# Optimization experiments

Measured on AMD Instinct MI355X. Metric: run time of the kernel, lower is better.

Reference implementation:

```python
import jax, jax.numpy as jnp
import numpy as np

B, T, F = 512, 98, 40
DIM, DEPTH, HEADS, DHEAD, MLP, NCLS = 192, 12, 3, 64, 768, 35
INNER = HEADS * DHEAD  # 192
N = T + 1  # cls token prepended
EPS = 1e-5


def _ln(x, g, b):
    m = jnp.mean(x, axis=-1, keepdims=True)
    v = jnp.mean(jnp.square(x - m), axis=-1, keepdims=True)
    return (x - m) * jax.lax.rsqrt(v + EPS) * g + b


def setup_inputs() -> dict:
    key = jax.random.key(0)
    ks = jax.random.split(key, 16)
    s = 0.02
    inp = {
        "img": jax.random.normal(ks[0], (B, T, F), jnp.float32),
        "lin_w": jax.random.normal(ks[1], (F, DIM), jnp.float32) * s,
        "g_feat": jax.random.normal(ks[2], (1, 1, DIM), jnp.float32),
        "pos_emb": jax.random.normal(ks[3], (1, N, DIM), jnp.float32),
        "ln1_g": jnp.ones((DEPTH, DIM), jnp.float32),
        "ln1_b": jnp.zeros((DEPTH, DIM), jnp.float32),
        "ln2_g": jnp.ones((DEPTH, DIM), jnp.float32),
        "ln2_b": jnp.zeros((DEPTH, DIM), jnp.float32),
        "qkv_w": jax.random.normal(ks[4], (DEPTH, DIM, 3 * INNER), jnp.float32) * s,
        "out_w": jax.random.normal(ks[5], (DEPTH, INNER, DIM), jnp.float32) * s,
        "out_b": jnp.zeros((DEPTH, DIM), jnp.float32),
        "ff1_w": jax.random.normal(ks[6], (DEPTH, DIM, MLP), jnp.float32) * s,
        "ff1_b": jnp.zeros((DEPTH, MLP), jnp.float32),
        "ff2_w": jax.random.normal(ks[7], (DEPTH, MLP, DIM), jnp.float32) * s,
        "ff2_b": jnp.zeros((DEPTH, DIM), jnp.float32),
        "head_ln_g": jnp.ones((DIM,), jnp.float32),
        "head_ln_b": jnp.zeros((DIM,), jnp.float32),
        "head_w": jax.random.normal(ks[8], (DIM, NCLS), jnp.float32) * s,
        "head_b": jnp.zeros((NCLS,), jnp.float32),
    }
    return inp


def reference(img, lin_w, g_feat, pos_emb, ln1_g, ln1_b, ln2_g, ln2_b,
              qkv_w, out_w, out_b, ff1_w, ff1_b, ff2_w, ff2_b,
              head_ln_g, head_ln_b, head_w, head_b):
    scale = DHEAD ** -0.5
    x = img @ lin_w  # [B, T, DIM]
    cls = jnp.broadcast_to(g_feat, (B, 1, DIM))
    x = jnp.concatenate([cls, x], axis=1) + pos_emb  # [B, N, DIM]

    for i in range(DEPTH):
        # --- attention (manual softmax, post-norm residual) ---
        qkv = x @ qkv_w[i]  # [B, N, 3*INNER]
        q, k, v = jnp.split(qkv, 3, axis=-1)
        rs = lambda t: t.reshape(B, N, HEADS, DHEAD).transpose(0, 2, 1, 3)
        q, k, v = rs(q), rs(k), rs(v)  # [B, H, N, D]
        dots = jnp.einsum('bhid,bhjd->bhij', q, k) * scale
        attn = jax.nn.softmax(dots, axis=-1)
        o = jnp.einsum('bhij,bhjd->bhid', attn, v)
        o = o.transpose(0, 2, 1, 3).reshape(B, N, INNER)
        o = o @ out_w[i] + out_b[i]
        x = _ln(o + x, ln1_g[i], ln1_b[i])
        # --- feedforward (exact GELU) ---
        h = jax.nn.gelu(x @ ff1_w[i] + ff1_b[i], approximate=False)
        f = h @ ff2_w[i] + ff2_b[i]
        x = _ln(f + x, ln2_g[i], ln2_b[i])

    x = x[:, 0]  # cls pooling
    x = _ln(x, head_ln_g, head_ln_b)
    return x @ head_w + head_b  # [B, NCLS]
```

## Files before the change

### kernel.cpp

```cpp
#include <hip/hip_runtime.h>

typedef unsigned short u16;

#define DIMM   192
#define DEPTH  12
#define NHEAD  3
#define MLPD   768
#define NCLS   35
#define NTOK   99
#define TIMG   98
#define FIMG   40
#define NBATCH 512
#define MT     7

#define XS_S 200
#define QH_S 72
#define VT_S 136
#define P_S  136
#define XS0  0
#define QH0  22400
#define KH0  30464
#define VT0  38528
#define P0   47232
#define RR_BYTE 124928
#define SMEM_BYTES 128512

typedef __attribute__((ext_vector_type(8))) __bf16 bf8;
typedef __attribute__((ext_vector_type(4))) float  f4;

__device__ __forceinline__ float b2f(u16 u){
  union { float f; unsigned u; } v; v.u = ((unsigned)u) << 16; return v.f;
}
__device__ __forceinline__ u16 f2b(float f){
  __bf16 h = (__bf16)f;
  union { __bf16 h; u16 u; } v; v.h = h;
  return v.u;
}
__device__ __forceinline__ f4 mm(bf8 a, bf8 b, f4 c){
  return __builtin_amdgcn_mfma_f32_16x16x32_bf16(a, b, c, 0, 0, 0);
}
__device__ __forceinline__ float gelu_f(float x){
  float z = x * 0.7071067811865476f;
  float az = fabsf(z);
  float t = 1.0f / (1.0f + 0.3275911f * az);
  float poly = ((((1.061405429f*t - 1.453152027f)*t + 1.421413741f)*t
                 - 0.284496736f)*t + 0.254829592f)*t;
  float erfv = 1.0f - poly * __expf(-az*az);
  erfv = (z < 0.0f) ? -erfv : erfv;
  return 0.5f * x * (1.0f + erfv);
}

extern "C" __global__ void permw(const float* __restrict__ src, u16* __restrict__ dst,
                                 int total, int KT, int NT, int realK, int Ndim){
  int i = blockIdx.x * 256 + threadIdx.x;
  if (i >= total) return;
  int j = i & 7, l = (i >> 3) & 63;
  int rest = i >> 9;
  int kt = rest % KT; rest /= KT;
  int nt = rest % NT; int layer = rest / NT;
  int k = kt*32 + (l>>4)*8 + j;
  int n = nt*16 + (l&15);
  float v = (k < realK) ? src[((size_t)layer*realK + k)*Ndim + n] : 0.0f;
  union { float f; unsigned u; } w; w.f = v;
  unsigned r = w.u + 0x7FFFu + ((w.u >> 16) & 1u);
  dst[i] = (u16)(r >> 16);
}

extern "C" __global__
__attribute__((amdgpu_flat_work_group_size(512,512), amdgpu_waves_per_eu(2,2)))
void vit_main(
    const float* __restrict__ img,   const float* __restrict__ g_feat,
    const float* __restrict__ pos_emb,
    const float* __restrict__ ln1_g, const float* __restrict__ ln1_b,
    const float* __restrict__ ln2_g, const float* __restrict__ ln2_b,
    const float* __restrict__ out_b, const float* __restrict__ ff1_b,
    const float* __restrict__ ff2_b,
    const float* __restrict__ hln_g, const float* __restrict__ hln_b,
    const float* __restrict__ head_w, const float* __restrict__ head_b,
    const u16* __restrict__ wlin, const u16* __restrict__ wqkv,
    const u16* __restrict__ wout, const u16* __restrict__ wff1,
    const u16* __restrict__ wff2,
    float* __restrict__ out)
{
  extern __shared__ __align__(16) u16 sm[];
  float* rowred = (float*)((char*)sm + RR_BYTE);
  const int tid  = threadIdx.x;
  const int lane = tid & 63;
  const int wv   = tid >> 6;
  const int wm   = wv >> 2;
  const int wn   = wv & 3;
  const int lg   = lane >> 4;
  const int lr   = lane & 15;
  const int b    = blockIdx.x;

  u16* const pA  = sm + XS0 + (wm*64 + lr)*XS_S + lg*8;
  u16* const pH  = sm + QH0 + (wm*64 + lr)*XS_S + lg*8;
  u16* const pOA = sm + QH0 + (wm*64 + lr)*QH_S + lg*8;
  u16* const pQS = sm + QH0 + (wm*64 + lg*4)*QH_S + wn*16 + lr;
  u16* const pVS = sm + VT0 + (wn*16 + lr)*VT_S + wm*64 + lg*4;
  u16* const pQA = sm + QH0 + (wv*16 + lr)*QH_S + lg*8;
  u16* const pKB = sm + KH0 + lr*QH_S + lg*8;
  u16* const pPS = sm + P0  + (wv*16 + lg*4)*P_S + lr;
  u16* const pPA = sm + P0  + (wv*16 + lr)*P_S + lg*8;
  u16* const pVB = sm + VT0 + lr*VT_S + lg*8;
  u16* const pOS = sm + QH0 + (wv*16 + lg*4)*QH_S + lr;
  u16* const pXE = sm + XS0 + (wm*64 + lg*4)*XS_S + wn*48 + lr;
  float* const pRR = rowred + (wm*64 + lg*4)*8;
  float* const pRS = pRR + wn*2;

  for (int i = tid; i < SMEM_BYTES/4; i += 512) ((unsigned*)sm)[i] = 0u;
  __syncthreads();

  const f4 zero4 = {0.f,0.f,0.f,0.f};

  auto epilogue_ln = [&](f4 (&acc)[4][3],
                         const float* gptr, const float* bptr, const float* biasptr){
    float gg[3], bb[3], ob[3];
#pragma unroll
    for (int nt = 0; nt < 3; ++nt) {
      int c = wn*48 + nt*16 + lr;
      gg[nt] = gptr[c]; bb[nt] = bptr[c]; ob[nt] = biasptr[c];
    }
#pragma unroll
    for (int mi = 0; mi < 4; ++mi) {
      if (mi < 3 || wm == 0) {
#pragma unroll
        for (int r = 0; r < 4; ++r) {
          float s1 = 0.f, s2 = 0.f;
#pragma unroll
          for (int nt = 0; nt < 3; ++nt) {
            float v = acc[mi][nt][r] + ob[nt] + b2f(pXE[(mi*16+r)*XS_S + nt*16]);
            acc[mi][nt][r] = v;
            s1 += v; s2 += v*v;
          }
          s1 += __shfl_xor(s1,1); s2 += __shfl_xor(s2,1);
          s1 += __shfl_xor(s1,2); s2 += __shfl_xor(s2,2);
          s1 += __shfl_xor(s1,4); s2 += __shfl_xor(s2,4);
          s1 += __shfl_xor(s1,8); s2 += __shfl_xor(s2,8);
          if (lr == 0) {
            pRS[(mi*16+r)*8 + 0] = s1;
            pRS[(mi*16+r)*8 + 1] = s2;
          }
        }
      }
    }
    __syncthreads();
#pragma unroll
    for (int mi = 0; mi < 4; ++mi) {
      if (mi < 3 || wm == 0) {
#pragma unroll
        for (int r = 0; r < 4; ++r) {
          float4 q0 = *(const float4*)&pRR[(mi*16+r)*8];
          float4 q1 = *(const float4*)&pRR[(mi*16+r)*8 + 4];
          float S1 = q0.x + q0.z + q1.x + q1.z;
          float S2 = q0.y + q0.w + q1.y + q1.w;
          float mean = S1 * (1.0f/DIMM);
          float var  = S2 * (1.0f/DIMM) - mean*mean;
          float rs = rsqrtf(var + 1e-5f);
          int row = wm*64 + mi*16 + lg*4 + r;
          if (row < NTOK) {
#pragma unroll
            for (int nt = 0; nt < 3; ++nt) {
              float y = (acc[mi][nt][r] - mean)*rs*gg[nt] + bb[nt];
              pXE[(mi*16+r)*XS_S + nt*16] = f2b(y);
            }
          }
        }
      }
    }
    __syncthreads();
  };

  const float* imgb = img + (size_t)b * (TIMG*FIMG);
  for (int i = tid; i < TIMG*FIMG; i += 512) {
    int r = i / FIMG, c = i - r*FIMG;
    sm[QH0 + (r+1)*QH_S + c] = f2b(imgb[i]);
  }
  __syncthreads();
  {
    const u16* wl = wlin + (size_t)(wn*3)*2*512 + lane*8;
    bf8 Bf[3][2];
#pragma unroll
    for (int nt = 0; nt < 3; ++nt)
#pragma unroll
      for (int kt = 0; kt < 2; ++kt)
        Bf[nt][kt] = *(const bf8*)&wl[(nt*2+kt)*512];
#pragma unroll
    for (int mi = 0; mi < 4; ++mi) {
      if (mi < 3 || wm == 0) {
        bf8 Af[2];
#pragma unroll
        for (int kt = 0; kt < 2; ++kt)
          Af[kt] = *(const bf8*)&pOA[mi*16*QH_S + kt*32];
#pragma unroll
        for (int nt = 0; nt < 3; ++nt) {
          f4 a = zero4;
#pragma unroll
          for (int kt = 0; kt < 2; ++kt) a = mm(Af[kt], Bf[nt][kt], a);
          int col = wn*48 + nt*16 + lr;
#pragma unroll
          for (int r = 0; r < 4; ++r) {
            int row = wm*64 + mi*16 + lg*4 + r;
            if (row < NTOK) {
              float v = a[r] + pos_emb[row*DIMM + col] + (row==0 ? g_feat[col] : 0.f);
              pXE[(mi*16+r)*XS_S + nt*16] = f2b(v);
            }
          }
        }
      }
    }
  }
  __syncthreads();

  for (int L = 0; L < DEPTH; ++L) {
    const u16* wq = wqkv + (size_t)L*36*6*512;
    f4 oacc[4][3];
#pragma unroll
    for (int mi = 0; mi < 4; ++mi)
#pragma unroll
      for (int nt = 0; nt < 3; ++nt) oacc[mi][nt] = zero4;

    for (int h = 0; h < NHEAD; ++h) {
      {
        const u16* wp = wq + ((size_t)(h*4 + wn)*6)*512 + lane*8;
        bf8 B[6];
#pragma unroll
        for (int kt = 0; kt < 6; ++kt) B[kt] = *(const bf8*)&wp[kt*512];
#pragma unroll
        for (int mi = 0; mi < 4; ++mi) {
          if (mi < 3 || wm == 0) {
            bf8 Af[6];
#pragma unroll
            for (int kt = 0; kt < 6; ++kt)
              Af[kt] = *(const bf8*)&pA[mi*16*XS_S + kt*32];
            f4 a = zero4;
#pragma unroll
            for (int kt = 0; kt < 6; ++kt) a = mm(Af[kt], B[kt], a);
#pragma unroll
            for (int r = 0; r < 4; ++r)
              pQS[(mi*16+r)*QH_S] = f2b(a[r]*0.125f);
          }
        }
      }
      {
        const u16* wp = wq + ((size_t)(12 + h*4 + wn)*6)*512 + lane*8;
        bf8 B[6];
#pragma unroll
        for (int kt = 0; kt < 6; ++kt) B[kt] = *(const bf8*)&wp[kt*512];
#pragma unroll
        for (int mi = 0; mi < 4; ++mi) {
          if (mi < 3 || wm == 0) {
            bf8 Af[6];
#pragma unroll
            for (int kt = 0; kt < 6; ++kt)
              Af[kt] = *(const bf8*)&pA[mi*16*XS_S + kt*32];
            f4 a = zero4;
#pragma unroll
            for (int kt = 0; kt < 6; ++kt) a = mm(Af[kt], B[kt], a);
#pragma unroll
            for (int r = 0; r < 4; ++r)
              pQS[(KH0-QH0) + (mi*16+r)*QH_S] = f2b(a[r]);
          }
        }
      }
      {
        const u16* wp = wq + ((size_t)(24 + h*4 + wn)*6)*512 + lane*8;
        bf8 B[6];
#pragma unroll
        for (int kt = 0; kt < 6; ++kt) B[kt] = *(const bf8*)&wp[kt*512];
#pragma unroll
        for (int mi = 0; mi < 4; ++mi) {
          if (mi < 3 || wm == 0) {
            bf8 Af[6];
#pragma unroll
            for (int kt = 0; kt < 6; ++kt)
              Af[kt] = *(const bf8*)&pA[mi*16*XS_S + kt*32];
            f4 a = zero4;
#pragma unroll
            for (int kt = 0; kt < 6; ++kt) a = mm(Af[kt], B[kt], a);
#pragma unroll
            for (int r = 0; r < 4; ++r)
              pVS[mi*16 + r] = f2b(a[r]);
          }
        }
      }
      __syncthreads();

      if (wv < MT) {
        bf8 Aq[2];
#pragma unroll
        for (int ks = 0; ks < 2; ++ks)
          Aq[ks] = *(const bf8*)&pQA[ks*32];
        f4 s[7];
#pragma unroll
        for (int kt = 0; kt < 7; ++kt) {
          f4 a = zero4;
#pragma unroll
          for (int ks = 0; ks < 2; ++ks) {
            bf8 Bk2 = *(const bf8*)&pKB[kt*16*QH_S + ks*32];
            a = mm(Aq[ks], Bk2, a);
          }
          s[kt] = a;
        }
#pragma unroll
        for (int r = 0; r < 4; ++r) {
          float m = s[0][r];
#pragma unroll
          for (int kt = 1; kt < 6; ++kt) m = fmaxf(m, s[kt][r]);
          m = fmaxf(m, (lr < 3) ? s[6][r] : -1e30f);
          m = fmaxf(m, __shfl_xor(m, 1));
          m = fmaxf(m, __shfl_xor(m, 2));
          m = fmaxf(m, __shfl_xor(m, 4));
          m = fmaxf(m, __shfl_xor(m, 8));
          float p[7]; float sum = 0.f;
#pragma unroll
          for (int kt = 0; kt < 6; ++kt) { p[kt] = __expf(s[kt][r] - m); sum += p[kt]; }
          p[6] = (lr < 3) ? __expf(s[6][r] - m) : 0.f;
          sum += p[6];
          sum += __shfl_xor(sum, 1);
          sum += __shfl_xor(sum, 2);
          sum += __shfl_xor(sum, 4);
          sum += __shfl_xor(sum, 8);
          float inv = 1.0f / sum;
#pragma unroll
          for (int kt = 0; kt < 7; ++kt)
            pPS[r*P_S + kt*16] = f2b(p[kt]*inv);
        }
        asm volatile("" ::: "memory");
        bf8 Ap[4];
#pragma unroll
        for (int ks = 0; ks < 4; ++ks)
          Ap[ks] = *(const bf8*)&pPA[ks*32];
#pragma unroll
        for (int nt = 0; nt < 4; ++nt) {
          f4 a = zero4;
#pragma unroll
          for (int ks = 0; ks < 4; ++ks) {
            bf8 Bv2 = *(const bf8*)&pVB[nt*16*VT_S + ks*32];
            a = mm(Ap[ks], Bv2, a);
          }
#pragma unroll
          for (int r = 0; r < 4; ++r)
            pOS[r*QH_S + nt*16] = f2b(a[r]);
        }
      }
      __syncthreads();

      {
        const u16* wp = wout + (((size_t)(L*12 + wn*3)*6) + h*2)*512 + lane*8;
        bf8 Bo[3][2];
#pragma unroll
        for (int nt = 0; nt < 3; ++nt)
#pragma unroll
          for (int ks = 0; ks < 2; ++ks)
            Bo[nt][ks] = *(const bf8*)&wp[(nt*6 + ks)*512];
#pragma unroll
        for (int mi = 0; mi < 4; ++mi) {
          if (mi < 3 || wm == 0) {
            bf8 Ao[2];
#pragma unroll
            for (int ks = 0; ks < 2; ++ks)
              Ao[ks] = *(const bf8*)&pOA[mi*16*QH_S + ks*32];
#pragma unroll
            for (int nt = 0; nt < 3; ++nt)
#pragma unroll
              for (int ks = 0; ks < 2; ++ks)
                oacc[mi][nt] = mm(Ao[ks], Bo[nt][ks], oacc[mi][nt]);
          }
        }
      }
      __syncthreads();
    }

    epilogue_ln(oacc, ln1_g + L*DIMM, ln1_b + L*DIMM, out_b + L*DIMM);

    f4 facc[4][3];
#pragma unroll
    for (int mi = 0; mi < 4; ++mi)
#pragma unroll
      for (int nt = 0; nt < 3; ++nt) facc[mi][nt] = zero4;

    for (int blk = 0; blk < 4; ++blk) {
      {
        const u16* wp = wff1 + ((size_t)(L*48 + blk*12 + wn*3)*6)*512 + lane*8;
        const float* fbp = ff1_b + L*MLPD + blk*192 + wn*48 + lr;
#pragma unroll
        for (int nt = 0; nt < 3; ++nt) {
          bf8 B[6];
#pragma unroll
          for (int kt = 0; kt < 6; ++kt) B[kt] = *(const bf8*)&wp[(nt*6+kt)*512];
          float fb = fbp[nt*16];
#pragma unroll
          for (int mi = 0; mi < 4; ++mi) {
            if (mi < 3 || wm == 0) {
              bf8 Af[6];
#pragma unroll
              for (int kt = 0; kt < 6; ++kt)
                Af[kt] = *(const bf8*)&pA[mi*16*XS_S + kt*32];
              f4 a = zero4;
#pragma unroll
              for (int kt = 0; kt < 6; ++kt) a = mm(Af[kt], B[kt], a);
#pragma unroll
              for (int r = 0; r < 4; ++r)
                pXE[(QH0-XS0) + (mi*16+r)*XS_S + nt*16] = f2b(gelu_f(a[r] + fb));
            }
          }
        }
      }
      __syncthreads();
      {
        const u16* wp = wff2 + ((size_t)(L*12 + wn*3)*24 + blk*6)*512 + lane*8;
#pragma unroll
        for (int nt = 0; nt < 3; ++nt) {
          bf8 B[6];
#pragma unroll
          for (int kt = 0; kt < 6; ++kt) B[kt] = *(const bf8*)&wp[(nt*24+kt)*512];
#pragma unroll
          for (int mi = 0; mi < 4; ++mi) {
            if (mi < 3 || wm == 0) {
              bf8 Ah[6];
#pragma unroll
              for (int kt = 0; kt < 6; ++kt)
                Ah[kt] = *(const bf8*)&pH[mi*16*XS_S + kt*32];
#pragma unroll
              for (int kt = 0; kt < 6; ++kt)
                facc[mi][nt] = mm(Ah[kt], B[kt], facc[mi][nt]);
            }
          }
        }
      }
      __syncthreads();
    }

    epilogue_ln(facc, ln2_g + L*DIMM, ln2_b + L*DIMM, ff2_b + L*DIMM);
  }

  float* yv = rowred;
  if (wv == 0) {
    float x0 = b2f(sm[XS0 + lane]);
    float x1 = b2f(sm[XS0 + 64 + lane]);
    float x2 = b2f(sm[XS0 + 128 + lane]);
    float s1 = x0+x1+x2;
    float s2 = x0*x0 + x1*x1 + x2*x2;
#pragma unroll
    for (int d = 1; d < 64; d <<= 1) { s1 += __shfl_xor(s1, d); s2 += __shfl_xor(s2, d); }
    float mean = s1*(1.0f/DIMM), var = s2*(1.0f/DIMM) - mean*mean;
    float rs = rsqrtf(var + 1e-5f);
    yv[lane]      = (x0-mean)*rs*hln_g[lane]      + hln_b[lane];
    yv[64+lane]   = (x1-mean)*rs*hln_g[64+lane]   + hln_b[64+lane];
    yv[128+lane]  = (x2-mean)*rs*hln_g[128+lane]  + hln_b[128+lane];
  }
  __syncthreads();
  if (tid < NCLS) {
    float acc = head_b[tid];
    for (int k = 0; k < DIMM; ++k) acc += yv[k] * head_w[k*NCLS + tid];
    out[(size_t)b*NCLS + tid] = acc;
  }
}

extern "C" void kernel_launch(void* const* d_in, const int* in_sizes, int n_in,
                              void* d_out, int out_size, void* d_ws, size_t ws_size,
                              hipStream_t stream) {
  const float* img    = (const float*)d_in[0];
  const float* lin_w  = (const float*)d_in[1];
  const float* g_feat = (const float*)d_in[2];
  const float* pos_emb= (const float*)d_in[3];
  const float* ln1_g  = (const float*)d_in[4];
  const float* ln1_b  = (const float*)d_in[5];
  const float* ln2_g  = (const float*)d_in[6];
  const float* ln2_b  = (const float*)d_in[7];
  const float* qkv_w  = (const float*)d_in[8];
  const float* out_w  = (const float*)d_in[9];
  const float* out_b  = (const float*)d_in[10];
  const float* ff1_w  = (const float*)d_in[11];
  const float* ff1_b  = (const float*)d_in[12];
  const float* ff2_w  = (const float*)d_in[13];
  const float* ff2_b  = (const float*)d_in[14];
  const float* hln_g  = (const float*)d_in[15];
  const float* hln_b  = (const float*)d_in[16];
  const float* head_w = (const float*)d_in[17];
  const float* head_b = (const float*)d_in[18];

  u16* ws   = (u16*)d_ws;
  u16* wlin = ws;
  u16* wqkv = wlin + 12288;
  u16* wout = wqkv + 1327104;
  u16* wff1 = wout + 442368;
  u16* wff2 = wff1 + 1769472;

  struct PermArgs { const float* src; u16* dst; int layers, Kdim, Ndim, realK; };
  const PermArgs pa[5] = {
    { lin_w, wlin, 1, 64, 192, 40 },
    { qkv_w, wqkv, 12, 192, 576, 192 },
    { out_w, wout, 12, 192, 192, 192 },
    { ff1_w, wff1, 12, 192, 768, 192 },
    { ff2_w, wff2, 12, 768, 192, 768 },
  };
  for (int i = 0; i < 5; ++i) {
    int total = pa[i].layers * (pa[i].Ndim/16) * (pa[i].Kdim/32) * 512;
    hipLaunchKernelGGL(permw, dim3((total + 255)/256), dim3(256), 0, stream,
                       pa[i].src, pa[i].dst, total, pa[i].Kdim/32, pa[i].Ndim/16,
                       pa[i].realK, pa[i].Ndim);
  }

  hipFuncSetAttribute(reinterpret_cast<const void*>(vit_main),
                      hipFuncAttributeMaxDynamicSharedMemorySize, SMEM_BYTES);

  hipLaunchKernelGGL(vit_main, dim3(NBATCH), dim3(512), SMEM_BYTES, stream,
                     img, g_feat, pos_emb, ln1_g, ln1_b, ln2_g, ln2_b,
                     out_b, ff1_b, ff2_b, hln_g, hln_b, head_w, head_b,
                     wlin, wqkv, wout, wff1, wff2, (float*)d_out);
}
```

Baseline: 1.573 ms.

## Split row tiles into two segments to cut accumulator register pressure

```diff
diff --git a/kernel.cpp b/kernel.cpp
--- a/kernel.cpp
+++ b/kernel.cpp
@@ -27,6 +27,7 @@
 
 typedef __attribute__((ext_vector_type(8))) __bf16 bf8;
 typedef __attribute__((ext_vector_type(4))) float  f4;
+typedef __attribute__((ext_vector_type(2))) unsigned u32x2;
 
 __device__ __forceinline__ float b2f(u16 u){
   union { float f; unsigned u; } v; v.u = ((unsigned)u) << 16; return v.f;
@@ -113,8 +114,8 @@
 
   const f4 zero4 = {0.f,0.f,0.f,0.f};
 
-  auto epilogue_ln = [&](f4 (&acc)[4][3],
-                         const float* gptr, const float* bptr, const float* biasptr){
+  auto epi_seg = [&](f4 (&acc)[2][3], int seg,
+                     const float* gptr, const float* bptr, const float* biasptr){
     float gg[3], bb[3], ob[3];
 #pragma unroll
     for (int nt = 0; nt < 3; ++nt) {
@@ -122,15 +123,16 @@
       gg[nt] = gptr[c]; bb[nt] = bptr[c]; ob[nt] = biasptr[c];
     }
 #pragma unroll
-    for (int mi = 0; mi < 4; ++mi) {
-      if (mi < 3 || wm == 0) {
+    for (int mi2 = 0; mi2 < 2; ++mi2) {
+      if (seg*2 + mi2 < 3 || wm == 0) {
 #pragma unroll
         for (int r = 0; r < 4; ++r) {
+          int ro = seg*32 + mi2*16 + r;
           float s1 = 0.f, s2 = 0.f;
 #pragma unroll
           for (int nt = 0; nt < 3; ++nt) {
-            float v = acc[mi][nt][r] + ob[nt] + b2f(pXE[(mi*16+r)*XS_S + nt*16]);
-            acc[mi][nt][r] = v;
+            float v = acc[mi2][nt][r] + ob[nt] + b2f(pXE[ro*XS_S + nt*16]);
+            acc[mi2][nt][r] = v;
             s1 += v; s2 += v*v;
           }
           s1 += __shfl_xor(s1,1); s2 += __shfl_xor(s2,1);
@@ -138,31 +140,32 @@
           s1 += __shfl_xor(s1,4); s2 += __shfl_xor(s2,4);
           s1 += __shfl_xor(s1,8); s2 += __shfl_xor(s2,8);
           if (lr == 0) {
-            pRS[(mi*16+r)*8 + 0] = s1;
-            pRS[(mi*16+r)*8 + 1] = s2;
+            pRS[ro*8 + 0] = s1;
+            pRS[ro*8 + 1] = s2;
           }
         }
       }
     }
     __syncthreads();
 #pragma unroll
-    for (int mi = 0; mi < 4; ++mi) {
-      if (mi < 3 || wm == 0) {
+    for (int mi2 = 0; mi2 < 2; ++mi2) {
+      if (seg*2 + mi2 < 3 || wm == 0) {
 #pragma unroll
         for (int r = 0; r < 4; ++r) {
-          float4 q0 = *(const float4*)&pRR[(mi*16+r)*8];
-          float4 q1 = *(const float4*)&pRR[(mi*16+r)*8 + 4];
+          int ro = seg*32 + mi2*16 + r;
+          float4 q0 = *(const float4*)&pRR[ro*8];
+          float4 q1 = *(const float4*)&pRR[ro*8 + 4];
           float S1 = q0.x + q0.z + q1.x + q1.z;
           float S2 = q0.y + q0.w + q1.y + q1.w;
           float mean = S1 * (1.0f/DIMM);
           float var  = S2 * (1.0f/DIMM) - mean*mean;
           float rs = rsqrtf(var + 1e-5f);
-          int row = wm*64 + mi*16 + lg*4 + r;
+          int row = wm*64 + ro + lg*4;
           if (row < NTOK) {
 #pragma unroll
             for (int nt = 0; nt < 3; ++nt) {
-              float y = (acc[mi][nt][r] - mean)*rs*gg[nt] + bb[nt];
-              pXE[(mi*16+r)*XS_S + nt*16] = f2b(y);
+              float y = (acc[mi2][nt][r] - mean)*rs*gg[nt] + bb[nt];
+              pXE[ro*XS_S + nt*16] = f2b(y);
             }
           }
         }
@@ -214,74 +217,71 @@
 
   for (int L = 0; L < DEPTH; ++L) {
     const u16* wq = wqkv + (size_t)L*36*6*512;
-    f4 oacc[4][3];
-#pragma unroll
-    for (int mi = 0; mi < 4; ++mi)
-#pragma unroll
-      for (int nt = 0; nt < 3; ++nt) oacc[mi][nt] = zero4;
+    f4 oacc0[2][3], oacc1[2][3];
+#pragma unroll
+    for (int mi2 = 0; mi2 < 2; ++mi2)
+#pragma unroll
+      for (int nt = 0; nt < 3; ++nt) { oacc0[mi2][nt] = zero4; oacc1[mi2][nt] = zero4; }
 
     for (int h = 0; h < NHEAD; ++h) {
-      {
-        const u16* wp = wq + ((size_t)(h*4 + wn)*6)*512 + lane*8;
-        bf8 B[6];
-#pragma unroll
-        for (int kt = 0; kt < 6; ++kt) B[kt] = *(const bf8*)&wp[kt*512];
-#pragma unroll
-        for (int mi = 0; mi < 4; ++mi) {
-          if (mi < 3 || wm == 0) {
+      const u16* wpq = wq + ((size_t)(      h*4 + wn)*6)*512 + lane*8;
+      const u16* wpk = wq + ((size_t)(12 + h*4 + wn)*6)*512 + lane*8;
+      const u16* wpv = wq + ((size_t)(24 + h*4 + wn)*6)*512 + lane*8;
+#pragma unroll
+      for (int seg = 0; seg < 2; ++seg) {
+#pragma unroll
+        for (int mi2 = 0; mi2 < 2; ++mi2) {
+          if (seg*2 + mi2 < 3 || wm == 0) {
+            const int ro = seg*32 + mi2*16;
             bf8 Af[6];
 #pragma unroll
             for (int kt = 0; kt < 6; ++kt)
-              Af[kt] = *(const bf8*)&pA[mi*16*XS_S + kt*32];
-            f4 a = zero4;
-#pragma unroll
-            for (int kt = 0; kt < 6; ++kt) a = mm(Af[kt], B[kt], a);
-#pragma unroll
-            for (int r = 0; r < 4; ++r)
-              pQS[(mi*16+r)*QH_S] = f2b(a[r]*0.125f);
-          }
-        }
-      }
-      {
-        const u16* wp = wq + ((size_t)(12 + h*4 + wn)*6)*512 + lane*8;
-        bf8 B[6];
-#pragma unroll
-        for (int kt = 0; kt < 6; ++kt) B[kt] = *(const bf8*)&wp[kt*512];
-#pragma unroll
-        for (int mi = 0; mi < 4; ++mi) {
-          if (mi < 3 || wm == 0) {
-            bf8 Af[6];
-#pragma unroll
-            for (int kt = 0; kt < 6; ++kt)
-              Af[kt] = *(const bf8*)&pA[mi*16*XS_S + kt*32];
-            f4 a = zero4;
-#pragma unroll
-            for (int kt = 0; kt < 6; ++kt) a = mm(Af[kt], B[kt], a);
-#pragma unroll
-            for (int r = 0; r < 4; ++r)
-              pQS[(KH0-QH0) + (mi*16+r)*QH_S] = f2b(a[r]);
-          }
-        }
-      }
-      {
-        const u16* wp = wq + ((size_t)(24 + h*4 + wn)*6)*512 + lane*8;
-        bf8 B[6];
-#pragma unroll
-        for (int kt = 0; kt < 6; ++kt) B[kt] = *(const bf8*)&wp[kt*512];
-#pragma unroll
-        for (int mi = 0; mi < 4; ++mi) {
-          if (mi < 3 || wm == 0) {
-            bf8 Af[6];
-#pragma unroll
-            for (int kt = 0; kt < 6; ++kt)
-              Af[kt] = *(const bf8*)&pA[mi*16*XS_S + kt*32];
-            f4 a = zero4;
-#pragma unroll
-            for (int kt = 0; kt < 6; ++kt) a = mm(Af[kt], B[kt], a);
-#pragma unroll
-            for (int r = 0; r < 4; ++r)
-              pVS[mi*16 + r] = f2b(a[r]);
-          }
+              Af[kt] = *(const bf8*)&pA[ro*XS_S + kt*32];
+            {
+              bf8 B[6];
+#pragma unroll
+              for (int kt = 0; kt < 6; ++kt) B[kt] = *(const bf8*)&wpq[kt*512];
+              f4 aA = zero4, aB = zero4;
+#pragma unroll
+              for (int k = 0; k < 3; ++k) aA = mm(Af[k], B[k], aA);
+#pragma unroll
+              for (int k = 0; k < 3; ++k) aB = mm(Af[3+k], B[3+k], aB);
+              f4 a = aA + aB;
+#pragma unroll
+              for (int r = 0; r < 4; ++r)
+                pQS[(ro+r)*QH_S] = f2b(a[r]*0.125f);
+            }
+            {
+              bf8 B[6];
+#pragma unroll
+              for (int kt = 0; kt < 6; ++kt) B[kt] = *(const bf8*)&wpk[kt*512];
+              f4 aA = zero4, aB = zero4;
+#pragma unroll
+              for (int k = 0; k < 3; ++k) aA = mm(Af[k], B[k], aA);
+#pragma unroll
+              for (int k = 0; k < 3; ++k) aB = mm(Af[3+k], B[3+k], aB);
+              f4 a = aA + aB;
+#pragma unroll
+              for (int r = 0; r < 4; ++r)
+                pQS[(KH0-QH0) + (ro+r)*QH_S] = f2b(a[r]);
+            }
+            {
+              bf8 B[6];
+#pragma unroll
+              for (int kt = 0; kt < 6; ++kt) B[kt] = *(const bf8*)&wpv[kt*512];
+              f4 aA = zero4, aB = zero4;
+#pragma unroll
+              for (int k = 0; k < 3; ++k) aA = mm(Af[k], B[k], aA);
+#pragma unroll
+              for (int k = 0; k < 3; ++k) aB = mm(Af[3+k], B[3+k], aB);
+              f4 a = aA + aB;
+              u32x2 pk;
+              pk.x = (unsigned)f2b(a[0]) | ((unsigned)f2b(a[1]) << 16);
+              pk.y = (unsigned)f2b(a[2]) | ((unsigned)f2b(a[3]) << 16);
+              *(u32x2*)(pVS + ro) = pk;
+            }
+          }
+          asm volatile("" ::: "memory");
         }
       }
       __syncthreads();
@@ -364,75 +364,88 @@
 #pragma unroll
             for (int nt = 0; nt < 3; ++nt)
 #pragma unroll
-              for (int ks = 0; ks < 2; ++ks)
-                oacc[mi][nt] = mm(Ao[ks], Bo[nt][ks], oacc[mi][nt]);
+              for (int ks = 0; ks < 2; ++ks) {
+                if (mi < 2) oacc0[mi  ][nt] = mm(Ao[ks], Bo[nt][ks], oacc0[mi  ][nt]);
+                else        oacc1[mi-2][nt] = mm(Ao[ks], Bo[nt][ks], oacc1[mi-2][nt]);
+              }
           }
         }
       }
       __syncthreads();
     }
 
-    epilogue_ln(oacc, ln1_g + L*DIMM, ln1_b + L*DIMM, out_b + L*DIMM);
-
-    f4 facc[4][3];
-#pragma unroll
-    for (int mi = 0; mi < 4; ++mi)
-#pragma unroll
-      for (int nt = 0; nt < 3; ++nt) facc[mi][nt] = zero4;
-
-    for (int blk = 0; blk < 4; ++blk) {
-      {
-        const u16* wp = wff1 + ((size_t)(L*48 + blk*12 + wn*3)*6)*512 + lane*8;
-        const float* fbp = ff1_b + L*MLPD + blk*192 + wn*48 + lr;
-#pragma unroll
-        for (int nt = 0; nt < 3; ++nt) {
-          bf8 B[6];
-#pragma unroll
-          for (int kt = 0; kt < 6; ++kt) B[kt] = *(const bf8*)&wp[(nt*6+kt)*512];
-          float fb = fbp[nt*16];
-#pragma unroll
-          for (int mi = 0; mi < 4; ++mi) {
-            if (mi < 3 || wm == 0) {
+    epi_seg(oacc0, 0, ln1_g + L*DIMM, ln1_b + L*DIMM, out_b + L*DIMM);
+    epi_seg(oacc1, 1, ln1_g + L*DIMM, ln1_b + L*DIMM, out_b + L*DIMM);
+
+#pragma unroll
+    for (int seg = 0; seg < 2; ++seg) {
+      f4 facc[2][3];
+#pragma unroll
+      for (int mi2 = 0; mi2 < 2; ++mi2)
+#pragma unroll
+        for (int nt = 0; nt < 3; ++nt) facc[mi2][nt] = zero4;
+
+      for (int blk = 0; blk < 4; ++blk) {
+        {
+          const u16* wp = wff1 + ((size_t)(L*48 + blk*12 + wn*3)*6)*512 + lane*8;
+          const float* fbp = ff1_b + L*MLPD + blk*192 + wn*48 + lr;
+#pragma unroll
+          for (int mi2 = 0; mi2 < 2; ++mi2) {
+            if (seg*2 + mi2 < 3 || wm == 0) {
+              const int ro = seg*32 + mi2*16;
               bf8 Af[6];
 #pragma unroll
               for (int kt = 0; kt < 6; ++kt)
-                Af[kt] = *(const bf8*)&pA[mi*16*XS_S + kt*32];
-              f4 a = zero4;
-#pragma unroll
-              for (int kt = 0; kt < 6; ++kt) a = mm(Af[kt], B[kt], a);
-#pragma unroll
-              for (int r = 0; r < 4; ++r)
-                pXE[(QH0-XS0) + (mi*16+r)*XS_S + nt*16] = f2b(gelu_f(a[r] + fb));
-            }
-          }
-        }
-      }
-      __syncthreads();
-      {
-        const u16* wp = wff2 + ((size_t)(L*12 + wn*3)*24 + blk*6)*512 + lane*8;
-#pragma unroll
-        for (int nt = 0; nt < 3; ++nt) {
-          bf8 B[6];
-#pragma unroll
-          for (int kt = 0; kt < 6; ++kt) B[kt] = *(const bf8*)&wp[(nt*24+kt)*512];
-#pragma unroll
-          for (int mi = 0; mi < 4; ++mi) {
-            if (mi < 3 || wm == 0) {
+                Af[kt] = *(const bf8*)&pA[ro*XS_S + kt*32];
+#pragma unroll
+              for (int nt = 0; nt < 3; ++nt) {
+                bf8 B[6];
+#pragma unroll
+                for (int kt = 0; kt < 6; ++kt) B[kt] = *(const bf8*)&wp[(nt*6+kt)*512];
+                float fb = fbp[nt*16];
+                f4 aA = zero4, aB = zero4;
+#pragma unroll
+                for (int k = 0; k < 3; ++k) aA = mm(Af[k], B[k], aA);
+#pragma unroll
+                for (int k = 0; k < 3; ++k) aB = mm(Af[3+k], B[3+k], aB);
+                f4 a = aA + aB;
+#pragma unroll
+                for (int r = 0; r < 4; ++r)
+                  pXE[(QH0-XS0) + (ro+r)*XS_S + nt*16] = f2b(gelu_f(a[r] + fb));
+                asm volatile("" ::: "memory");
+              }
+            }
+          }
+        }
+        __syncthreads();
+        {
+          const u16* wp = wff2 + ((size_t)(L*12 + wn*3)*24 + blk*6)*512 + lane*8;
+#pragma unroll
+          for (int mi2 = 0; mi2 < 2; ++mi2) {
+            if (seg*2 + mi2 < 3 || wm == 0) {
+              const int ro = seg*32 + mi2*16;
               bf8 Ah[6];
 #pragma unroll
               for (int kt = 0; kt < 6; ++kt)
-                Ah[kt] = *(const bf8*)&pH[mi*16*XS_S + kt*32];
-#pragma unroll
-              for (int kt = 0; kt < 6; ++kt)
-                facc[mi][nt] = mm(Ah[kt], B[kt], facc[mi][nt]);
-            }
-          }
-        }
-      }
-      __syncthreads();
+                Ah[kt] = *(const bf8*)&pH[ro*XS_S + kt*32];
+#pragma unroll
+              for (int nt = 0; nt < 3; ++nt) {
+                bf8 B[6];
+#pragma unroll
+                for (int kt = 0; kt < 6; ++kt) B[kt] = *(const bf8*)&wp[(nt*24+kt)*512];
+#pragma unroll
+                for (int kt = 0; kt < 6; ++kt)
+                  facc[mi2][nt] = mm(Ah[kt], B[kt], facc[mi2][nt]);
+                asm volatile("" ::: "memory");
+              }
+            }
+          }
+        }
+        __syncthreads();
+      }
+
+      epi_seg(facc, seg, ln2_g + L*DIMM, ln2_b + L*DIMM, ff2_b + L*DIMM);
     }
-
-    epilogue_ln(facc, ln2_g + L*DIMM, ln2_b + L*DIMM, ff2_b + L*DIMM);
   }
 
   float* yv = rowred;
```

After: 1.995 ms. 26.8% more time.

## Double workgroup to 1024 threads, halve per-wave row tiles, split MFMA chains

Applied to the files above, without the earlier changes.

```diff
diff --git a/kernel.cpp b/kernel.cpp
--- a/kernel.cpp
+++ b/kernel.cpp
@@ -27,6 +27,7 @@
 
 typedef __attribute__((ext_vector_type(8))) __bf16 bf8;
 typedef __attribute__((ext_vector_type(4))) float  f4;
+typedef __attribute__((ext_vector_type(2))) unsigned u32x2;
 
 __device__ __forceinline__ float b2f(u16 u){
   union { float f; unsigned u; } v; v.u = ((unsigned)u) << 16; return v.f;
@@ -67,7 +68,7 @@
 }
 
 extern "C" __global__
-__attribute__((amdgpu_flat_work_group_size(512,512), amdgpu_waves_per_eu(2,2)))
+__attribute__((amdgpu_flat_work_group_size(1024,1024), amdgpu_waves_per_eu(4,4)))
 void vit_main(
     const float* __restrict__ img,   const float* __restrict__ g_feat,
     const float* __restrict__ pos_emb,
@@ -93,27 +94,27 @@
   const int lr   = lane & 15;
   const int b    = blockIdx.x;
 
-  u16* const pA  = sm + XS0 + (wm*64 + lr)*XS_S + lg*8;
-  u16* const pH  = sm + QH0 + (wm*64 + lr)*XS_S + lg*8;
-  u16* const pOA = sm + QH0 + (wm*64 + lr)*QH_S + lg*8;
-  u16* const pQS = sm + QH0 + (wm*64 + lg*4)*QH_S + wn*16 + lr;
-  u16* const pVS = sm + VT0 + (wn*16 + lr)*VT_S + wm*64 + lg*4;
+  u16* const pA  = sm + XS0 + (wm*32 + lr)*XS_S + lg*8;
+  u16* const pH  = sm + QH0 + (wm*32 + lr)*XS_S + lg*8;
+  u16* const pOA = sm + QH0 + (wm*32 + lr)*QH_S + lg*8;
+  u16* const pQS = sm + QH0 + (wm*32 + lg*4)*QH_S + wn*16 + lr;
+  u16* const pVS = sm + VT0 + (wn*16 + lr)*VT_S + wm*32 + lg*4;
   u16* const pQA = sm + QH0 + (wv*16 + lr)*QH_S + lg*8;
   u16* const pKB = sm + KH0 + lr*QH_S + lg*8;
   u16* const pPS = sm + P0  + (wv*16 + lg*4)*P_S + lr;
   u16* const pPA = sm + P0  + (wv*16 + lr)*P_S + lg*8;
   u16* const pVB = sm + VT0 + lr*VT_S + lg*8;
   u16* const pOS = sm + QH0 + (wv*16 + lg*4)*QH_S + lr;
-  u16* const pXE = sm + XS0 + (wm*64 + lg*4)*XS_S + wn*48 + lr;
-  float* const pRR = rowred + (wm*64 + lg*4)*8;
+  u16* const pXE = sm + XS0 + (wm*32 + lg*4)*XS_S + wn*48 + lr;
+  float* const pRR = rowred + (wm*32 + lg*4)*8;
   float* const pRS = pRR + wn*2;
 
-  for (int i = tid; i < SMEM_BYTES/4; i += 512) ((unsigned*)sm)[i] = 0u;
+  for (int i = tid; i < SMEM_BYTES/4; i += 1024) ((unsigned*)sm)[i] = 0u;
   __syncthreads();
 
   const f4 zero4 = {0.f,0.f,0.f,0.f};
 
-  auto epilogue_ln = [&](f4 (&acc)[4][3],
+  auto epilogue_ln = [&](f4 (&acc)[2][3],
                          const float* gptr, const float* bptr, const float* biasptr){
     float gg[3], bb[3], ob[3];
 #pragma unroll
@@ -122,14 +123,15 @@
       gg[nt] = gptr[c]; bb[nt] = bptr[c]; ob[nt] = biasptr[c];
     }
 #pragma unroll
-    for (int mi = 0; mi < 4; ++mi) {
-      if (mi < 3 || wm == 0) {
+    for (int mi = 0; mi < 2; ++mi) {
+      if (wm < 3 || mi == 0) {
 #pragma unroll
         for (int r = 0; r < 4; ++r) {
+          int ro = mi*16 + r;
           float s1 = 0.f, s2 = 0.f;
 #pragma unroll
           for (int nt = 0; nt < 3; ++nt) {
-            float v = acc[mi][nt][r] + ob[nt] + b2f(pXE[(mi*16+r)*XS_S + nt*16]);
+            float v = acc[mi][nt][r] + ob[nt] + b2f(pXE[ro*XS_S + nt*16]);
             acc[mi][nt][r] = v;
             s1 += v; s2 += v*v;
           }
@@ -138,31 +140,32 @@
           s1 += __shfl_xor(s1,4); s2 += __shfl_xor(s2,4);
           s1 += __shfl_xor(s1,8); s2 += __shfl_xor(s2,8);
           if (lr == 0) {
-            pRS[(mi*16+r)*8 + 0] = s1;
-            pRS[(mi*16+r)*8 + 1] = s2;
+            pRS[ro*8 + 0] = s1;
+            pRS[ro*8 + 1] = s2;
           }
         }
       }
     }
     __syncthreads();
 #pragma unroll
-    for (int mi = 0; mi < 4; ++mi) {
-      if (mi < 3 || wm == 0) {
+    for (int mi = 0; mi < 2; ++mi) {
+      if (wm < 3 || mi == 0) {
 #pragma unroll
         for (int r = 0; r < 4; ++r) {
-          float4 q0 = *(const float4*)&pRR[(mi*16+r)*8];
-          float4 q1 = *(const float4*)&pRR[(mi*16+r)*8 + 4];
+          int ro = mi*16 + r;
+          float4 q0 = *(const float4*)&pRR[ro*8];
+          float4 q1 = *(const float4*)&pRR[ro*8 + 4];
           float S1 = q0.x + q0.z + q1.x + q1.z;
           float S2 = q0.y + q0.w + q1.y + q1.w;
           float mean = S1 * (1.0f/DIMM);
           float var  = S2 * (1.0f/DIMM) - mean*mean;
           float rs = rsqrtf(var + 1e-5f);
-          int row = wm*64 + mi*16 + lg*4 + r;
+          int row = wm*32 + ro + lg*4;
           if (row < NTOK) {
 #pragma unroll
             for (int nt = 0; nt < 3; ++nt) {
               float y = (acc[mi][nt][r] - mean)*rs*gg[nt] + bb[nt];
-              pXE[(mi*16+r)*XS_S + nt*16] = f2b(y);
+              pXE[ro*XS_S + nt*16] = f2b(y);
             }
           }
         }
@@ -172,7 +175,7 @@
   };
 
   const float* imgb = img + (size_t)b * (TIMG*FIMG);
-  for (int i = tid; i < TIMG*FIMG; i += 512) {
+  for (int i = tid; i < TIMG*FIMG; i += 1024) {
     int r = i / FIMG, c = i - r*FIMG;
     sm[QH0 + (r+1)*QH_S + c] = f2b(imgb[i]);
   }
@@ -186,8 +189,8 @@
       for (int kt = 0; kt < 2; ++kt)
         Bf[nt][kt] = *(const bf8*)&wl[(nt*2+kt)*512];
 #pragma unroll
-    for (int mi = 0; mi < 4; ++mi) {
-      if (mi < 3 || wm == 0) {
+    for (int mi = 0; mi < 2; ++mi) {
+      if (wm < 3 || mi == 0) {
         bf8 Af[2];
 #pragma unroll
         for (int kt = 0; kt < 2; ++kt)
@@ -200,7 +203,7 @@
           int col = wn*48 + nt*16 + lr;
 #pragma unroll
           for (int r = 0; r < 4; ++r) {
-            int row = wm*64 + mi*16 + lg*4 + r;
+            int row = wm*32 + mi*16 + lg*4 + r;
             if (row < NTOK) {
               float v = a[r] + pos_emb[row*DIMM + col] + (row==0 ? g_feat[col] : 0.f);
               pXE[(mi*16+r)*XS_S + nt*16] = f2b(v);
@@ -214,9 +217,9 @@
 
   for (int L = 0; L < DEPTH; ++L) {
     const u16* wq = wqkv + (size_t)L*36*6*512;
-    f4 oacc[4][3];
-#pragma unroll
-    for (int mi = 0; mi < 4; ++mi)
+    f4 oacc[2][3];
+#pragma unroll
+    for (int mi = 0; mi < 2; ++mi)
 #pragma unroll
       for (int nt = 0; nt < 3; ++nt) oacc[mi][nt] = zero4;
 
@@ -227,15 +230,18 @@
 #pragma unroll
         for (int kt = 0; kt < 6; ++kt) B[kt] = *(const bf8*)&wp[kt*512];
 #pragma unroll
-        for (int mi = 0; mi < 4; ++mi) {
-          if (mi < 3 || wm == 0) {
+        for (int mi = 0; mi < 2; ++mi) {
+          if (wm < 3 || mi == 0) {
             bf8 Af[6];
 #pragma unroll
             for (int kt = 0; kt < 6; ++kt)
               Af[kt] = *(const bf8*)&pA[mi*16*XS_S + kt*32];
-            f4 a = zero4;
-#pragma unroll
-            for (int kt = 0; kt < 6; ++kt) a = mm(Af[kt], B[kt], a);
+            f4 aA = zero4, aB = zero4;
+#pragma unroll
+            for (int k = 0; k < 3; ++k) aA = mm(Af[k], B[k], aA);
+#pragma unroll
+            for (int k = 0; k < 3; ++k) aB = mm(Af[3+k], B[3+k], aB);
+            f4 a = aA + aB;
 #pragma unroll
             for (int r = 0; r < 4; ++r)
               pQS[(mi*16+r)*QH_S] = f2b(a[r]*0.125f);
@@ -248,15 +254,18 @@
 #pragma unroll
         for (int kt = 0; kt < 6; ++kt) B[kt] = *(const bf8*)&wp[kt*512];
 #pragma unroll
-        for (int mi = 0; mi < 4; ++mi) {
-          if (mi < 3 || wm == 0) {
+        for (int mi = 0; mi < 2; ++mi) {
+          if (wm < 3 || mi == 0) {
             bf8 Af[6];
 #pragma unroll
             for (int kt = 0; kt < 6; ++kt)
               Af[kt] = *(const bf8*)&pA[mi*16*XS_S + kt*32];
-            f4 a = zero4;
-#pragma unroll
-            for (int kt = 0; kt < 6; ++kt) a = mm(Af[kt], B[kt], a);
+            f4 aA = zero4, aB = zero4;
+#pragma unroll
+            for (int k = 0; k < 3; ++k) aA = mm(Af[k], B[k], aA);
+#pragma unroll
+            for (int k = 0; k < 3; ++k) aB = mm(Af[3+k], B[3+k], aB);
+            f4 a = aA + aB;
 #pragma unroll
             for (int r = 0; r < 4; ++r)
               pQS[(KH0-QH0) + (mi*16+r)*QH_S] = f2b(a[r]);
@@ -269,18 +278,22 @@
 #pragma unroll
         for (int kt = 0; kt < 6; ++kt) B[kt] = *(const bf8*)&wp[kt*512];
 #pragma unroll
-        for (int mi = 0; mi < 4; ++mi) {
-          if (mi < 3 || wm == 0) {
+        for (int mi = 0; mi < 2; ++mi) {
+          if (wm < 3 || mi == 0) {
             bf8 Af[6];
 #pragma unroll
             for (int kt = 0; kt < 6; ++kt)
               Af[kt] = *(const bf8*)&pA[mi*16*XS_S + kt*32];
-            f4 a = zero4;
-#pragma unroll
-            for (int kt = 0; kt < 6; ++kt) a = mm(Af[kt], B[kt], a);
-#pragma unroll
-            for (int r = 0; r < 4; ++r)
-              pVS[mi*16 + r] = f2b(a[r]);
+            f4 aA = zero4, aB = zero4;
+#pragma unroll
+            for (int k = 0; k < 3; ++k) aA = mm(Af[k], B[k], aA);
+#pragma unroll
+            for (int k = 0; k < 3; ++k) aB = mm(Af[3+k], B[3+k], aB);
+            f4 a = aA + aB;
+            u32x2 pk;
+            pk.x = (unsigned)f2b(a[0]) | ((unsigned)f2b(a[1]) << 16);
+            pk.y = (unsigned)f2b(a[2]) | ((unsigned)f2b(a[3]) << 16);
+            *(u32x2*)(pVS + mi*16) = pk;
           }
         }
       }
@@ -355,8 +368,8 @@
           for (int ks = 0; ks < 2; ++ks)
             Bo[nt][ks] = *(const bf8*)&wp[(nt*6 + ks)*512];
 #pragma unroll
-        for (int mi = 0; mi < 4; ++mi) {
-          if (mi < 3 || wm == 0) {
+        for (int mi = 0; mi < 2; ++mi) {
+          if (wm < 3 || mi == 0) {
             bf8 Ao[2];
 #pragma unroll
             for (int ks = 0; ks < 2; ++ks)
@@ -374,9 +387,9 @@
 
     epilogue_ln(oacc, ln1_g + L*DIMM, ln1_b + L*DIMM, out_b + L*DIMM);
 
-    f4 facc[4][3];
-#pragma unroll
-    for (int mi = 0; mi < 4; ++mi)
+    f4 facc[2][3];
+#pragma unroll
+    for (int mi = 0; mi < 2; ++mi)
 #pragma unroll
       for (int nt = 0; nt < 3; ++nt) facc[mi][nt] = zero4;
 
@@ -391,15 +404,18 @@
           for (int kt = 0; kt < 6; ++kt) B[kt] = *(const bf8*)&wp[(nt*6+kt)*512];
           float fb = fbp[nt*16];
 #pragma unroll
-          for (int mi = 0; mi < 4; ++mi) {
-            if (mi < 3 || wm == 0) {
+          for (int mi = 0; mi < 2; ++mi) {
+            if (wm < 3 || mi == 0) {
               bf8 Af[6];
 #pragma unroll
               for (int kt = 0; kt < 6; ++kt)
                 Af[kt] = *(const bf8*)&pA[mi*16*XS_S + kt*32];
-              f4 a = zero4;
-#pragma unroll
-              for (int kt = 0; kt < 6; ++kt) a = mm(Af[kt], B[kt], a);
+              f4 aA = zero4, aB = zero4;
+#pragma unroll
+              for (int k = 0; k < 3; ++k) aA = mm(Af[k], B[k], aA);
+#pragma unroll
+              for (int k = 0; k < 3; ++k) aB = mm(Af[3+k], B[3+k], aB);
+              f4 a = aA + aB;
 #pragma unroll
               for (int r = 0; r < 4; ++r)
                 pXE[(QH0-XS0) + (mi*16+r)*XS_S + nt*16] = f2b(gelu_f(a[r] + fb));
@@ -416,8 +432,8 @@
 #pragma unroll
           for (int kt = 0; kt < 6; ++kt) B[kt] = *(const bf8*)&wp[(nt*24+kt)*512];
 #pragma unroll
-          for (int mi = 0; mi < 4; ++mi) {
-            if (mi < 3 || wm == 0) {
+          for (int mi = 0; mi < 2; ++mi) {
+            if (wm < 3 || mi == 0) {
               bf8 Ah[6];
 #pragma unroll
               for (int kt = 0; kt < 6; ++kt)
@@ -506,7 +522,7 @@
   hipFuncSetAttribute(reinterpret_cast<const void*>(vit_main),
                       hipFuncAttributeMaxDynamicSharedMemorySize, SMEM_BYTES);
 
-  hipLaunchKernelGGL(vit_main, dim3(NBATCH), dim3(512), SMEM_BYTES, stream,
+  hipLaunchKernelGGL(vit_main, dim3(NBATCH), dim3(1024), SMEM_BYTES, stream,
                      img, g_feat, pos_emb, ln1_g, ln1_b, ln2_g, ln2_b,
                      out_b, ff1_b, ff2_b, hln_g, hln_b, head_w, head_b,
                      wlin, wqkv, wout, wff1, wff2, (float*)d_out);
```

Result: faster. 1.517 ms (-3.6%).
